# Performance work log

Hardware: AMD Instinct MI355X
Metric: run time of the kernel (lower is better)

## Reference

```python
import jax, jax.numpy as jnp
import numpy as np

K = 9          # neighbors per node (loop=False)
BN_EPS = 1e-5  # BatchNorm2d eps


def setup_inputs() -> dict:
    key = jax.random.key(0)
    k1, k2, k3 = jax.random.split(key, 3)
    B, C, H, W_ = 16, 384, 32, 32
    x = jax.random.normal(k1, (B, C, H, W_), dtype=jnp.float32)
    # GCNConv linear weight (PyG stores [out, in]; y = x @ W.T) and bias
    Wg = jax.random.normal(k2, (C, C), dtype=jnp.float32) / np.sqrt(C)
    bg = jax.random.normal(k3, (C,), dtype=jnp.float32) * 0.02
    gamma = jnp.ones((C,), dtype=jnp.float32)
    beta = jnp.zeros((C,), dtype=jnp.float32)
    return {"x": x, "Wg": Wg, "bg": bg, "gamma": gamma, "beta": beta}


def _knn_indices(xn):
    # xn: [B, N, C] -> neighbor indices [B, N, K] (self excluded)
    sq = jnp.sum(xn * xn, axis=-1)                       # [B, N]
    d = sq[:, :, None] + sq[:, None, :] - 2.0 * jnp.einsum("bnc,bmc->bnm", xn, xn)
    N = xn.shape[1]
    d = d + jnp.eye(N, dtype=xn.dtype) * jnp.finfo(xn.dtype).max  # exclude self
    _, nbr = jax.lax.top_k(-d, K)                        # [B, N, K]
    return nbr


def reference(x, Wg, bg, gamma, beta):
    B, C, H, W_ = x.shape
    N = H * W_
    BN_nodes = B * N
    shortcut = x

    # Flatten to nodes: [B*N, C]
    xn = jnp.transpose(x, (0, 2, 3, 1)).reshape(B, N, C)

    # Per-graph kNN in feature space (PyG knn_graph, flow source_to_target:
    # edges from neighbor (src) to query node (dst))
    nbr = _knn_indices(xn)                                # [B, N, K]
    offs = (jnp.arange(B) * N)[:, None, None]             # [B,1,1]
    src = (nbr + offs).reshape(-1)                        # [B*N*K]
    dst = jnp.broadcast_to(jnp.arange(N)[None, :, None] + offs, (B, N, K)).reshape(-1)

    # GCNConv: add self loops, symmetric normalization
    loops = jnp.arange(BN_nodes)
    src = jnp.concatenate([src, loops])
    dst = jnp.concatenate([dst, loops])

    xw = xn.reshape(BN_nodes, C) @ Wg.T                   # node-wise linear

    deg = jax.ops.segment_sum(jnp.ones_like(dst, dtype=xw.dtype), dst, num_segments=BN_nodes)
    dinv = jax.lax.rsqrt(deg)                             # deg >= 1 due to self loops
    norm = dinv[src] * dinv[dst]                          # [E]

    out = jax.ops.segment_sum(norm[:, None] * xw[src], dst, num_segments=BN_nodes) + bg

    # Back to B x C x H x W
    out = jnp.transpose(out.reshape(B, H, W_, C), (0, 3, 1, 2))

    # BatchNorm2d (training-mode batch statistics, biased variance)
    mu = jnp.mean(out, axis=(0, 2, 3), keepdims=True)
    var = jnp.mean((out - mu) ** 2, axis=(0, 2, 3), keepdims=True)
    out = gamma[None, :, None, None] * (out - mu) * jax.lax.rsqrt(var + BN_EPS) + beta[None, :, None, None]

    # GELU + residual (drop_path = 0 -> identity)
    out = jax.nn.gelu(out) + shortcut
    return out
```

## Files before the change

kernel.cpp:

```cpp
#include <hip/hip_runtime.h>
#include <math.h>

#define B_ 16
#define C_ 384
#define N_ 1024
#define K_ 9

typedef _Float16 f16x8 __attribute__((ext_vector_type(8)));
typedef _Float16 f16x4 __attribute__((ext_vector_type(4)));
typedef float f32x4 __attribute__((ext_vector_type(4)));
typedef unsigned long long u64;

__device__ __forceinline__ void gld_lds16(const void* g, void* l) {
  __builtin_amdgcn_global_load_lds((const __attribute__((address_space(1))) void*)g,
                                   (__attribute__((address_space(3))) void*)l, 16, 0, 0);
}

__global__ void k_cvt(const float* __restrict__ x, ushort* __restrict__ xhT,
                      ushort* __restrict__ xlT) {
  const int bid = blockIdx.x;
  const int ct = bid % 12;
  const int nt = (bid / 12) & 15;
  const int b = bid / 192;
  const int c0 = ct * 32, n0 = nt * 64;
  __shared__ float ld[32 * 65];
  const int t = threadIdx.x;
  {
    const int c = t >> 3, n8 = (t & 7) * 8;
    const float* src = x + ((size_t)(b * C_ + c0 + c) * N_ + n0 + n8);
    float4 v0 = *(const float4*)src;
    float4 v1 = *(const float4*)(src + 4);
    float vv[8] = {v0.x, v0.y, v0.z, v0.w, v1.x, v1.y, v1.z, v1.w};
#pragma unroll
    for (int j = 0; j < 8; ++j) ld[c * 65 + n8 + j] = vv[j];
  }
  __syncthreads();
  {
    const int n = t >> 2, c8 = (t & 3) * 8;
    f16x8 hv, lv;
#pragma unroll
    for (int j = 0; j < 8; ++j) {
      float v = ld[(c8 + j) * 65 + n];
      _Float16 h = (_Float16)v;
      _Float16 l = (_Float16)(v - (float)h);
      hv[j] = h;
      lv[j] = l;
    }
    const size_t off = (size_t)(b * N_ + n0 + n) * C_ + c0 + c8;
    *(f16x8*)(xhT + off) = hv;
    *(f16x8*)(xlT + off) = lv;
  }
}

__global__ void k_cvtw(const float* __restrict__ Wg, ushort* __restrict__ WgH,
                       ushort* __restrict__ WgL) {
  const int i = (blockIdx.x * 256 + threadIdx.x) * 4;
  float4 v = *(const float4*)(Wg + i);
  float vv[4] = {v.x, v.y, v.z, v.w};
  f16x4 hv, lv;
#pragma unroll
  for (int j = 0; j < 4; ++j) {
    _Float16 h = (_Float16)vv[j];
    hv[j] = h;
    lv[j] = (_Float16)(vv[j] - (float)h);
  }
  *(f16x4*)(WgH + i) = hv;
  *(f16x4*)(WgL + i) = lv;
}

__global__ void k_sq1(const float* __restrict__ x, double* __restrict__ part) {
  const int bid = blockIdx.x;
  const int b = bid >> 6, q = (bid >> 2) & 15, nt = bid & 3;
  const int n = nt * 256 + threadIdx.x;
  const float* xb = x + ((size_t)b * C_ + q * 24) * N_ + n;
  double s = 0.0;
#pragma unroll 4
  for (int c = 0; c < 24; ++c) {
    float v = xb[(size_t)c * N_];
    s = fma((double)v, (double)v, s);
  }
  part[((size_t)b * 16 + q) * N_ + n] = s;
}

__global__ void k_sq2(const double* __restrict__ part, float* __restrict__ sq) {
  const int idx = blockIdx.x * blockDim.x + threadIdx.x;
  const int b = idx >> 10, n = idx & 1023;
  const double* p = part + (size_t)b * 16 * N_ + n;
  double s = 0.0;
#pragma unroll
  for (int q = 0; q < 16; ++q) s += p[(size_t)q * N_];
  sq[idx] = (float)s;
}

__global__ __launch_bounds__(256, 2) void k_gram(const ushort* __restrict__ xhT,
                                                 const ushort* __restrict__ xlT,
                                                 const float* __restrict__ sq,
                                                 float* __restrict__ D, int base_b, int nb) {
  const int bid = blockIdx.x;
  int b_local, pid;
  if (nb >= 8) {
    const int x = bid & 7, j = bid >> 3, grp = nb >> 3;
    b_local = x * grp + (j >> 6);
    pid = j & 63;
  } else {
    b_local = bid >> 6;
    pid = bid & 63;
  }
  const int b = base_b + b_local;
  const int rt = pid >> 3, mt = pid & 7;
  const int n0 = rt * 128, m0 = mt * 128;

  __shared__ alignas(16) char sm[2][32768];
  const int t = threadIdx.x;
  const int lane = t & 63, wid = t >> 6, quad = lane >> 4, lrow = lane & 15;
  const int wr = wid >> 1, wc = wid & 1;
  const int lrow4 = lane >> 2, lpos = lane & 3;

  const char* src = (const char*)((wid & 1) ? xlT : xhT) +
                    (size_t)(b * N_ + ((wid >> 1) ? m0 : n0)) * C_ * 2;

  f32x4 acc[4][4];
#pragma unroll
  for (int mi = 0; mi < 4; ++mi)
#pragma unroll
    for (int ni = 0; ni < 4; ++ni) acc[mi][ni] = (f32x4){0.f, 0.f, 0.f, 0.f};

  auto stage = [&](int it) {
    char* dst = sm[it & 1] + wid * 8192;
    const int ktB = it * 64;
#pragma unroll
    for (int i = 0; i < 8; ++i) {
      const int row = i * 16 + lrow4;
      const int swz = lpos ^ ((row >> 1) & 3);
      gld_lds16(src + (size_t)row * 768 + ktB + swz * 16, dst + i * 1024 + lane * 16);
    }
  };

  stage(0);
  for (int it = 0; it < 12; ++it) {
    __syncthreads();
    if (it < 11) stage(it + 1);
    const char* smb = sm[it & 1];
    f16x8 ah[4], al[4];
#pragma unroll
    for (int mi = 0; mi < 4; ++mi) {
      const int row = wr * 64 + mi * 16 + lrow;
      const int off = row * 64 + (quad ^ ((row >> 1) & 3)) * 16;
      ah[mi] = *(const f16x8*)(smb + off);
      al[mi] = *(const f16x8*)(smb + 8192 + off);
    }
#pragma unroll
    for (int ni = 0; ni < 4; ++ni) {
      const int row = wc * 64 + ni * 16 + lrow;
      const int off = row * 64 + (quad ^ ((row >> 1) & 3)) * 16;
      f16x8 bh = *(const f16x8*)(smb + 16384 + off);
      f16x8 bl = *(const f16x8*)(smb + 24576 + off);
#pragma unroll
      for (int mi = 0; mi < 4; ++mi) {
        acc[mi][ni] = __builtin_amdgcn_mfma_f32_16x16x32_f16(ah[mi], bh, acc[mi][ni], 0, 0, 0);
        acc[mi][ni] = __builtin_amdgcn_mfma_f32_16x16x32_f16(al[mi], bh, acc[mi][ni], 0, 0, 0);
        acc[mi][ni] = __builtin_amdgcn_mfma_f32_16x16x32_f16(ah[mi], bl, acc[mi][ni], 0, 0, 0);
      }
    }
  }

  const float* sqb = sq + b * N_;
  float sqm[4];
#pragma unroll
  for (int ni = 0; ni < 4; ++ni) sqm[ni] = sqb[m0 + wc * 64 + ni * 16 + lrow];
  float sqn_[4][4];
#pragma unroll
  for (int mi = 0; mi < 4; ++mi)
#pragma unroll
    for (int r = 0; r < 4; ++r) sqn_[mi][r] = sqb[n0 + wr * 64 + mi * 16 + quad * 4 + r];

  float* Db = D + (size_t)b_local * N_ * N_;
#pragma unroll
  for (int mi = 0; mi < 4; ++mi)
#pragma unroll
    for (int ni = 0; ni < 4; ++ni)
#pragma unroll
      for (int r = 0; r < 4; ++r) {
        const int ng = n0 + wr * 64 + mi * 16 + quad * 4 + r;
        const int mg = m0 + wc * 64 + ni * 16 + lrow;
        float d = fmaf(-2.f, acc[mi][ni][r], sqn_[mi][r] + sqm[ni]);
        if (ng == mg) d = 3.402823466e38f;
        Db[(size_t)ng * N_ + mg] = d;
      }
}

__device__ __forceinline__ void ce2f(float& a, float& b) {
  float lo = fminf(a, b), hi = fmaxf(a, b);
  a = lo;
  b = hi;
}

__global__ __launch_bounds__(256) void k_scan(const float* __restrict__ D,
                                              int* __restrict__ nbr, int base_node) {
  const int t = threadIdx.x;
  const int lane = t & 63, wid = t >> 6;
  const int g = lane >> 5;
  const int ll = lane & 31;
  const int nl = blockIdx.x * 8 + wid * 2 + g;
  const float* row = D + (size_t)nl * N_ + ll * 32;
  float v[32];
#pragma unroll
  for (int i = 0; i < 8; ++i) {
    float4 q = *(const float4*)(row + i * 4);
    v[i * 4 + 0] = q.x;
    v[i * 4 + 1] = q.y;
    v[i * 4 + 2] = q.z;
    v[i * 4 + 3] = q.w;
  }
  float key[9];
#pragma unroll
  for (int k = 0; k < 9; ++k) key[k] = 3.402823466e38f;
#pragma unroll
  for (int j = 0; j < 32; ++j) {
    key[8] = fminf(key[8], v[j]);
#pragma unroll
    for (int s = 8; s >= 1; --s) ce2f(key[s - 1], key[s]);
  }
#pragma unroll
  for (int lvl = 1; lvl < 32; lvl <<= 1) {
    float pk[9];
#pragma unroll
    for (int k = 0; k < 9; ++k) pk[k] = __shfl_xor(key[k], lvl, 64);
    float m[9];
#pragma unroll
    for (int k = 0; k < 9; ++k) m[k] = fminf(key[k], pk[8 - k]);
    ce2f(m[0], m[8]);
    ce2f(m[1], m[5]); ce2f(m[2], m[6]); ce2f(m[3], m[7]); ce2f(m[4], m[8]);
    ce2f(m[1], m[3]); ce2f(m[2], m[4]); ce2f(m[5], m[7]); ce2f(m[6], m[8]);
    ce2f(m[1], m[2]); ce2f(m[3], m[4]); ce2f(m[5], m[6]); ce2f(m[7], m[8]);
#pragma unroll
    for (int k = 0; k < 9; ++k) key[k] = m[k];
  }
  const float v9 = key[8];
  int c_lt = 0;
#pragma unroll
  for (int k = 0; k < 8; ++k) c_lt += (key[k] < v9) ? 1 : 0;

  unsigned lt_mask = 0u, eq_mask = 0u;
#pragma unroll
  for (int j = 0; j < 32; ++j) {
    lt_mask |= (v[j] < v9) ? (1u << j) : 0u;
    eq_mask |= (v[j] == v9) ? (1u << j) : 0u;
  }
  const int lt_cnt = __popc(lt_mask), eq_cnt = __popc(eq_mask);
  int packed = lt_cnt | (eq_cnt << 16);
  int run = packed;
#pragma unroll
  for (int off = 1; off < 32; off <<= 1) {
    int q = __shfl_up(run, off, 32);
    if (ll >= off) run += q;
  }
  const int pref = run - packed;
  const int lt_pref = pref & 0xFFFF, eq_pref = pref >> 16;

  int* np = nbr + (size_t)(base_node + nl) * K_;
  int slot = lt_pref;
  unsigned m = lt_mask;
  while (m) {
    int j = __builtin_ctz(m);
    m &= m - 1;
    np[slot++] = ll * 32 + j;
  }
  slot = c_lt + eq_pref;
  m = eq_mask;
  while (m && slot < 9) {
    int j = __builtin_ctz(m);
    m &= m - 1;
    np[slot++] = ll * 32 + j;
  }
}

__global__ __launch_bounds__(256, 3) void k_xw(const ushort* __restrict__ xhT,
                                               const ushort* __restrict__ xlT,
                                               const ushort* __restrict__ WgH,
                                               const ushort* __restrict__ WgL,
                                               float* __restrict__ xw) {
  const int bid = blockIdx.x;
  const int xcd = bid & 7, j = bid >> 3;
  const int pair = xcd * 16 + j / 6;
  const int ct = j % 6;
  const int b = pair >> 3, nt = pair & 7;
  const int co0 = ct * 64, n0 = nt * 128;
  __shared__ alignas(16) char sm[2][24576];
  const int t = threadIdx.x;
  const int lane = t & 63, wid = t >> 6, quad = lane >> 4, lrow = lane & 15;
  const int wr = wid >> 1, wc = wid & 1;
  const int lrow4 = lane >> 2, lpos = lane & 3;

  f32x4 acc[2][4];
#pragma unroll
  for (int mi = 0; mi < 2; ++mi)
#pragma unroll
    for (int ni = 0; ni < 4; ++ni) acc[mi][ni] = (f32x4){0.f, 0.f, 0.f, 0.f};

  const char* asrc[2] = {(const char*)(WgH + (size_t)co0 * C_),
                         (const char*)(WgL + (size_t)co0 * C_)};
  const char* bsrc[2] = {(const char*)(xhT + (size_t)(b * N_ + n0) * C_),
                         (const char*)(xlT + (size_t)(b * N_ + n0) * C_)};

  auto stage = [&](int it) {
    char* dst = sm[it & 1];
    const int ktB = it * 64;
#pragma unroll
    for (int i = 0; i < 6; ++i) {
      const int c = wid * 6 + i;
      const char* src;
      int base, row;
      if (c < 8) {
        const int arr = c >> 2, sub = c & 3;
        src = asrc[arr];
        base = arr * 4096 + sub * 1024;
        row = sub * 16 + lrow4;
      } else {
        const int cc = c - 8, arr = cc >> 3, sub = cc & 7;
        src = bsrc[arr];
        base = 8192 + arr * 8192 + sub * 1024;
        row = sub * 16 + lrow4;
      }
      const int swz = lpos ^ ((row >> 1) & 3);
      gld_lds16(src + (size_t)row * 768 + ktB + swz * 16, dst + base + lane * 16);
    }
  };

  stage(0);
  for (int it = 0; it < 12; ++it) {
    __syncthreads();
    if (it < 11) stage(it + 1);
    const char* smb = sm[it & 1];
    f16x8 bh[4], bl[4];
#pragma unroll
    for (int ni = 0; ni < 4; ++ni) {
      const int row = wr * 64 + ni * 16 + lrow;
      const int off = row * 64 + (quad ^ ((row >> 1) & 3)) * 16;
      bh[ni] = *(const f16x8*)(smb + 8192 + off);
      bl[ni] = *(const f16x8*)(smb + 16384 + off);
    }
#pragma unroll
    for (int mi = 0; mi < 2; ++mi) {
      const int row = wc * 32 + mi * 16 + lrow;
      const int off = row * 64 + (quad ^ ((row >> 1) & 3)) * 16;
      f16x8 ah = *(const f16x8*)(smb + off);
      f16x8 al = *(const f16x8*)(smb + 4096 + off);
#pragma unroll
      for (int ni = 0; ni < 4; ++ni) {
        acc[mi][ni] = __builtin_amdgcn_mfma_f32_16x16x32_f16(ah, bh[ni], acc[mi][ni], 0, 0, 0);
        acc[mi][ni] = __builtin_amdgcn_mfma_f32_16x16x32_f16(al, bh[ni], acc[mi][ni], 0, 0, 0);
        acc[mi][ni] = __builtin_amdgcn_mfma_f32_16x16x32_f16(ah, bl[ni], acc[mi][ni], 0, 0, 0);
      }
    }
  }
#pragma unroll
  for (int mi = 0; mi < 2; ++mi)
#pragma unroll
    for (int ni = 0; ni < 4; ++ni)
#pragma unroll
      for (int r = 0; r < 4; ++r) {
        const int c_g = co0 + wc * 32 + mi * 16 + quad * 4 + r;
        const int n_g = n0 + wr * 64 + ni * 16 + lrow;
        xw[((size_t)b * C_ + c_g) * N_ + n_g] = acc[mi][ni][r];
      }
}

__global__ __launch_bounds__(256) void k_agg(const float* __restrict__ xw,
                                             const int* __restrict__ nbr,
                                             const float* __restrict__ bg,
                                             float* __restrict__ out,
                                             float* __restrict__ stats) {
  const int ct = blockIdx.x % (C_ / 8);
  const int b = blockIdx.x / (C_ / 8);
  const int c0 = ct * 8;
  __shared__ alignas(16) int nb_l[N_ * K_];
  __shared__ alignas(16) float row_l[8][N_ + 4];
  __shared__ float red[2][8][4];
  const int tid = threadIdx.x;
  const int4* gp = (const int4*)(nbr + (size_t)b * N_ * K_);
  int4* lp = (int4*)nb_l;
  for (int t = tid; t < N_ * K_ / 4; t += 256) lp[t] = gp[t];
  for (int t = tid; t < 8 * (N_ / 4); t += 256) {
    const int j = t >> 8, n4 = t & 255;
    float4 v = ((const float4*)(xw + ((size_t)(b * C_ + c0 + j)) * N_))[n4];
    *(float4*)&row_l[j][n4 * 4] = v;
  }
  __syncthreads();
  float bgc[8];
#pragma unroll
  for (int j = 0; j < 8; ++j) bgc[j] = bg[c0 + j];
  float s1[8], s2[8];
#pragma unroll
  for (int j = 0; j < 8; ++j) {
    s1[j] = 0.f;
    s2[j] = 0.f;
  }
  float* outb = out + ((size_t)b * C_ + c0) * N_;
#pragma unroll
  for (int s = 0; s < 4; ++s) {
    const int n = tid + 256 * s;
    const int* nn_ = &nb_l[n * K_];
    int idx[K_];
#pragma unroll
    for (int k = 0; k < K_; ++k) idx[k] = nn_[k];
    float a[8];
#pragma unroll
    for (int j = 0; j < 8; ++j) a[j] = row_l[j][n];
#pragma unroll
    for (int k = 0; k < K_; ++k) {
      const int m = idx[k];
#pragma unroll
      for (int j = 0; j < 8; ++j) a[j] += row_l[j][m];
    }
#pragma unroll
    for (int j = 0; j < 8; ++j) {
      float y = fmaf(a[j], 0.099999994f, bgc[j]);
      outb[(size_t)j * N_ + n] = y;
      s1[j] += y;
      s2[j] = fmaf(y, y, s2[j]);
    }
  }
#pragma unroll
  for (int off = 32; off > 0; off >>= 1)
#pragma unroll
    for (int j = 0; j < 8; ++j) {
      s1[j] += __shfl_down(s1[j], off, 64);
      s2[j] += __shfl_down(s2[j], off, 64);
    }
  const int lane = tid & 63, wid = tid >> 6;
  if (lane == 0)
#pragma unroll
    for (int j = 0; j < 8; ++j) {
      red[0][j][wid] = s1[j];
      red[1][j][wid] = s2[j];
    }
  __syncthreads();
  if (tid < 16) {
    const int j = tid & 7, which = tid >> 3;
    float v = red[which][j][0] + red[which][j][1] + red[which][j][2] + red[which][j][3];
    atomicAdd(&stats[which * C_ + c0 + j], v);
  }
}

__global__ void k_bn(const float* __restrict__ x, const float* __restrict__ gamma,
                     const float* __restrict__ beta, const float* __restrict__ stats,
                     float* __restrict__ out) {
  const int f = blockIdx.x * blockDim.x + threadIdx.x;
  const int e = f * 4;
  const int c = (e >> 10) % C_;
  const float inv = 1.f / 16384.f;
  const float mu = stats[c] * inv;
  const float var = fmaf(-mu, mu, stats[C_ + c] * inv);
  const float sc = gamma[c] * rsqrtf(var + 1e-5f);
  const float sh = fmaf(-mu, sc, beta[c]);
  float4 y = ((const float4*)out)[f];
  float4 xv = ((const float4*)x)[f];
  auto gl = [](float z) {
    float z3 = z * z * z;
    float t = 0.7978845608028654f * fmaf(0.044715f, z3, z);
    float th = tanhf(t);
    return 0.5f * z * (1.f + th);
  };
  float4 o;
  o.x = gl(fmaf(y.x, sc, sh)) + xv.x;
  o.y = gl(fmaf(y.y, sc, sh)) + xv.y;
  o.z = gl(fmaf(y.z, sc, sh)) + xv.z;
  o.w = gl(fmaf(y.w, sc, sh)) + xv.w;
  ((float4*)out)[f] = o;
}

extern "C" void kernel_launch(void* const* d_in, const int* in_sizes, int n_in,
                              void* d_out, int out_size, void* d_ws, size_t ws_size,
                              hipStream_t stream) {
  const float* x = (const float*)d_in[0];
  const float* Wg = (const float*)d_in[1];
  const float* bg = (const float*)d_in[2];
  const float* gamma = (const float*)d_in[3];
  const float* beta = (const float*)d_in[4];
  float* out = (float*)d_out;

  int nb;
  if (ws_size >= 94000000) nb = 16;
  else if (ws_size >= 60500000) nb = 8;
  else nb = 4;

  char* ws = (char*)d_ws;
  ushort* xhT = (ushort*)ws;
  ushort* xlT = (ushort*)(ws + 12582912);
  ushort* WgH = (ushort*)(ws + 25165824);
  ushort* WgL = (ushort*)(ws + 25460736);
  float* sq = (float*)(ws + 25755648);
  float* Dbuf = (float*)(ws + 25821184);
  float* xw = (float*)(ws + 25821184);
  double* sqpart = (double*)(ws + 25821184);
  size_t dreg = (size_t)nb * 4194304;
  if (dreg < 25165824) dreg = 25165824;
  int* nbr = (int*)(ws + 25821184 + dreg);
  float* stats = (float*)(ws + 25821184 + dreg + 589824);

  hipMemsetAsync(stats, 0, 2 * C_ * sizeof(float), stream);
  k_cvt<<<3072, 256, 0, stream>>>(x, xhT, xlT);
  k_cvtw<<<144, 256, 0, stream>>>(Wg, WgH, WgL);
  k_sq1<<<1024, 256, 0, stream>>>(x, sqpart);
  k_sq2<<<64, 256, 0, stream>>>(sqpart, sq);
  for (int r = 0; r < B_ / nb; ++r) {
    k_gram<<<nb * 64, 256, 0, stream>>>(xhT, xlT, sq, Dbuf, r * nb, nb);
    k_scan<<<nb * 128, 256, 0, stream>>>(Dbuf, nbr, r * nb * N_);
  }
  k_xw<<<768, 256, 0, stream>>>(xhT, xlT, WgH, WgL, xw);
  k_agg<<<B_ * (C_ / 8), 256, 0, stream>>>(xw, nbr, bg, out, stats);
  k_bn<<<6144, 256, 0, stream>>>(x, gamma, beta, stats, out);
}
```

Baseline: 219.5 us.

## Fuse kNN top-k selection into gram kernel epilogue with per-tile partial merge

Instead of writing the full dense NxN distance matrix to global memory and rescanning it, the gram kernel now transposes its MFMA outputs, stages each 128x128 distance tile in LDS with a swizzle, and computes a per-tile top-9 per query row there. It writes packed (monotone-float, index) 64-bit candidates, 72 per node, and a small merge kernel reduces those to the final 9 neighbours. This removes the large global write and read of the distance matrix, and the batch-chunking loop now always processes all 16 graphs in one launch. The cost is extra LDS work and a serial top-k in the gram epilogue. The merge kernel runs only 64 blocks, so it has low parallelism.

```diff
diff --git a/kernel.cpp b/kernel.cpp
--- a/kernel.cpp
+++ b/kernel.cpp
@@ -92,10 +92,22 @@
   sq[idx] = (float)s;
 }
 
+__device__ __forceinline__ void ce2f(float& a, float& b) {
+  float lo = fminf(a, b), hi = fmaxf(a, b);
+  a = lo;
+  b = hi;
+}
+__device__ __forceinline__ void ce9u(u64& a, u64& b) {
+  u64 lo = a < b ? a : b;
+  u64 hi = a < b ? b : a;
+  a = lo;
+  b = hi;
+}
+
 __global__ __launch_bounds__(256, 2) void k_gram(const ushort* __restrict__ xhT,
                                                  const ushort* __restrict__ xlT,
                                                  const float* __restrict__ sq,
-                                                 float* __restrict__ D, int base_b, int nb) {
+                                                 u64* __restrict__ part, int base_b, int nb) {
   const int bid = blockIdx.x;
   int b_local, pid;
   if (nb >= 8) {
@@ -157,75 +169,72 @@
       f16x8 bl = *(const f16x8*)(smb + 24576 + off);
 #pragma unroll
       for (int mi = 0; mi < 4; ++mi) {
-        acc[mi][ni] = __builtin_amdgcn_mfma_f32_16x16x32_f16(ah[mi], bh, acc[mi][ni], 0, 0, 0);
-        acc[mi][ni] = __builtin_amdgcn_mfma_f32_16x16x32_f16(al[mi], bh, acc[mi][ni], 0, 0, 0);
-        acc[mi][ni] = __builtin_amdgcn_mfma_f32_16x16x32_f16(ah[mi], bl, acc[mi][ni], 0, 0, 0);
+        acc[mi][ni] = __builtin_amdgcn_mfma_f32_16x16x32_f16(bh, ah[mi], acc[mi][ni], 0, 0, 0);
+        acc[mi][ni] = __builtin_amdgcn_mfma_f32_16x16x32_f16(bh, al[mi], acc[mi][ni], 0, 0, 0);
+        acc[mi][ni] = __builtin_amdgcn_mfma_f32_16x16x32_f16(bl, ah[mi], acc[mi][ni], 0, 0, 0);
       }
     }
   }
+  __syncthreads();
 
   const float* sqb = sq + b * N_;
-  float sqm[4];
-#pragma unroll
-  for (int ni = 0; ni < 4; ++ni) sqm[ni] = sqb[m0 + wc * 64 + ni * 16 + lrow];
-  float sqn_[4][4];
-#pragma unroll
-  for (int mi = 0; mi < 4; ++mi)
-#pragma unroll
-    for (int r = 0; r < 4; ++r) sqn_[mi][r] = sqb[n0 + wr * 64 + mi * 16 + quad * 4 + r];
-
-  float* Db = D + (size_t)b_local * N_ * N_;
-#pragma unroll
-  for (int mi = 0; mi < 4; ++mi)
-#pragma unroll
-    for (int ni = 0; ni < 4; ++ni)
+  float sqm_[4][4];
+#pragma unroll
+  for (int ni = 0; ni < 4; ++ni)
+#pragma unroll
+    for (int r = 0; r < 4; ++r) sqm_[ni][r] = sqb[m0 + wc * 64 + ni * 16 + quad * 4 + r];
+  float sqq_[4];
+#pragma unroll
+  for (int mi = 0; mi < 4; ++mi) sqq_[mi] = sqb[n0 + wr * 64 + mi * 16 + lrow];
+
+  float* smf = (float*)sm;
+#pragma unroll
+  for (int mi = 0; mi < 4; ++mi) {
+    const int qL = wr * 64 + mi * 16 + lrow;
+    const int qG = n0 + qL;
+#pragma unroll
+    for (int ni = 0; ni < 4; ++ni) {
+      const int tc = wc * 16 + ni * 4 + quad;
+      const int stv = tc ^ (qL & 31);
+      f32x4 dv;
 #pragma unroll
       for (int r = 0; r < 4; ++r) {
-        const int ng = n0 + wr * 64 + mi * 16 + quad * 4 + r;
-        const int mg = m0 + wc * 64 + ni * 16 + lrow;
-        float d = fmaf(-2.f, acc[mi][ni][r], sqn_[mi][r] + sqm[ni]);
-        if (ng == mg) d = 3.402823466e38f;
-        Db[(size_t)ng * N_ + mg] = d;
+        const int mG = m0 + wc * 64 + ni * 16 + quad * 4 + r;
+        float d = fmaf(-2.f, acc[mi][ni][r], sqq_[mi] + sqm_[ni][r]);
+        if (mG == qG) d = 3.402823466e38f;
+        dv[r] = d;
       }
-}
-
-__device__ __forceinline__ void ce2f(float& a, float& b) {
-  float lo = fminf(a, b), hi = fmaxf(a, b);
-  a = lo;
-  b = hi;
-}
-
-__global__ __launch_bounds__(256) void k_scan(const float* __restrict__ D,
-                                              int* __restrict__ nbr, int base_node) {
-  const int t = threadIdx.x;
-  const int lane = t & 63, wid = t >> 6;
-  const int g = lane >> 5;
-  const int ll = lane & 31;
-  const int nl = blockIdx.x * 8 + wid * 2 + g;
-  const float* row = D + (size_t)nl * N_ + ll * 32;
-  float v[32];
-#pragma unroll
-  for (int i = 0; i < 8; ++i) {
-    float4 q = *(const float4*)(row + i * 4);
-    v[i * 4 + 0] = q.x;
-    v[i * 4 + 1] = q.y;
-    v[i * 4 + 2] = q.z;
-    v[i * 4 + 3] = q.w;
+      *(f32x4*)(smf + qL * 128 + stv * 4) = dv;
+    }
+  }
+  __syncthreads();
+
+  const int qsel = wid * 32 + (lane & 31);
+  const int half = lane >> 5;
+  float v[64];
+#pragma unroll
+  for (int i = 0; i < 16; ++i) {
+    const int tc = half * 16 + i;
+    const int stv = tc ^ (qsel & 31);
+    f32x4 q4 = *(const f32x4*)(smf + qsel * 128 + stv * 4);
+    v[i * 4 + 0] = q4[0];
+    v[i * 4 + 1] = q4[1];
+    v[i * 4 + 2] = q4[2];
+    v[i * 4 + 3] = q4[3];
   }
   float key[9];
 #pragma unroll
   for (int k = 0; k < 9; ++k) key[k] = 3.402823466e38f;
 #pragma unroll
-  for (int j = 0; j < 32; ++j) {
+  for (int j = 0; j < 64; ++j) {
     key[8] = fminf(key[8], v[j]);
 #pragma unroll
     for (int s = 8; s >= 1; --s) ce2f(key[s - 1], key[s]);
   }
-#pragma unroll
-  for (int lvl = 1; lvl < 32; lvl <<= 1) {
+  {
     float pk[9];
 #pragma unroll
-    for (int k = 0; k < 9; ++k) pk[k] = __shfl_xor(key[k], lvl, 64);
+    for (int k = 0; k < 9; ++k) pk[k] = __shfl_xor(key[k], 32, 64);
     float m[9];
 #pragma unroll
     for (int k = 0; k < 9; ++k) m[k] = fminf(key[k], pk[8 - k]);
@@ -241,38 +250,58 @@
 #pragma unroll
   for (int k = 0; k < 8; ++k) c_lt += (key[k] < v9) ? 1 : 0;
 
-  unsigned lt_mask = 0u, eq_mask = 0u;
-#pragma unroll
-  for (int j = 0; j < 32; ++j) {
-    lt_mask |= (v[j] < v9) ? (1u << j) : 0u;
-    eq_mask |= (v[j] == v9) ? (1u << j) : 0u;
-  }
-  const int lt_cnt = __popc(lt_mask), eq_cnt = __popc(eq_mask);
-  int packed = lt_cnt | (eq_cnt << 16);
-  int run = packed;
-#pragma unroll
-  for (int off = 1; off < 32; off <<= 1) {
-    int q = __shfl_up(run, off, 32);
-    if (ll >= off) run += q;
-  }
-  const int pref = run - packed;
-  const int lt_pref = pref & 0xFFFF, eq_pref = pref >> 16;
-
+  u64 lt_mask = 0ull, eq_mask = 0ull;
+#pragma unroll
+  for (int j = 0; j < 64; ++j) {
+    lt_mask |= (v[j] < v9) ? (1ull << j) : 0ull;
+    eq_mask |= (v[j] == v9) ? (1ull << j) : 0ull;
+  }
+  const int ltc = __popcll(lt_mask), eqc = __popcll(eq_mask);
+  const int packed = ltc | (eqc << 16);
+  const int other = __shfl_xor(packed, 32, 64);
+  const int lt_pref = half ? (other & 0xFFFF) : 0;
+  const int eq_pref = half ? (other >> 16) : 0;
+
+  u64* pp = part + ((size_t)(b_local * N_ + n0 + qsel) * 8 + mt) * 9;
+  int slot = lt_pref;
+  u64 msk = lt_mask;
+  while (msk) {
+    const int j = __builtin_ctzll(msk);
+    msk &= msk - 1;
+    const int mL = half * 64 + j;
+    const int stv = (mL >> 2) ^ (qsel & 31);
+    const float val = smf[qsel * 128 + stv * 4 + (mL & 3)];
+    unsigned fb = __float_as_uint(val);
+    unsigned mono = (fb >> 31) ? ~fb : (fb | 0x80000000u);
+    pp[slot++] = ((u64)mono << 32) | (unsigned)(m0 + mL);
+  }
+  unsigned fb9 = __float_as_uint(v9);
+  unsigned mono9 = (fb9 >> 31) ? ~fb9 : (fb9 | 0x80000000u);
+  slot = c_lt + eq_pref;
+  msk = eq_mask;
+  while (msk && slot < 9) {
+    const int j = __builtin_ctzll(msk);
+    msk &= msk - 1;
+    pp[slot++] = ((u64)mono9 << 32) | (unsigned)(m0 + half * 64 + j);
+  }
+}
+
+__global__ void k_mrg(const u64* __restrict__ part, int* __restrict__ nbr, int base_node) {
+  const int nl = blockIdx.x * 256 + threadIdx.x;
+  const u64* p = part + (size_t)nl * 72;
+  u64 key[9];
+#pragma unroll
+  for (int k = 0; k < 9; ++k) key[k] = ~0ull;
+#pragma unroll 4
+  for (int j = 0; j < 72; ++j) {
+    u64 kk = p[j];
+    key[8] = key[8] < kk ? key[8] : kk;
+#pragma unroll
+    for (int s = 8; s >= 1; --s) ce9u(key[s - 1], key[s]);
+  }
   int* np = nbr + (size_t)(base_node + nl) * K_;
-  int slot = lt_pref;
-  unsigned m = lt_mask;
-  while (m) {
-    int j = __builtin_ctz(m);
-    m &= m - 1;
-    np[slot++] = ll * 32 + j;
-  }
-  slot = c_lt + eq_pref;
-  m = eq_mask;
-  while (m && slot < 9) {
-    int j = __builtin_ctz(m);
-    m &= m - 1;
-    np[slot++] = ll * 32 + j;
-  }
+#pragma unroll
+  for (int k = 0; k < 9; ++k) np[k] = (int)(unsigned)(key[k] & 0xFFFFFFFFu);
 }
 
 __global__ __launch_bounds__(256, 3) void k_xw(const ushort* __restrict__ xhT,
@@ -480,10 +509,7 @@
   const float* beta = (const float*)d_in[4];
   float* out = (float*)d_out;
 
-  int nb;
-  if (ws_size >= 94000000) nb = 16;
-  else if (ws_size >= 60500000) nb = 8;
-  else nb = 4;
+  const int nb = 16;
 
   char* ws = (char*)d_ws;
   ushort* xhT = (ushort*)ws;
@@ -491,11 +517,10 @@
   ushort* WgH = (ushort*)(ws + 25165824);
   ushort* WgL = (ushort*)(ws + 25460736);
   float* sq = (float*)(ws + 25755648);
-  float* Dbuf = (float*)(ws + 25821184);
+  u64* part = (u64*)(ws + 25821184);
   float* xw = (float*)(ws + 25821184);
   double* sqpart = (double*)(ws + 25821184);
-  size_t dreg = (size_t)nb * 4194304;
-  if (dreg < 25165824) dreg = 25165824;
+  size_t dreg = 25165824;
   int* nbr = (int*)(ws + 25821184 + dreg);
   float* stats = (float*)(ws + 25821184 + dreg + 589824);
 
@@ -504,10 +529,8 @@
   k_cvtw<<<144, 256, 0, stream>>>(Wg, WgH, WgL);
   k_sq1<<<1024, 256, 0, stream>>>(x, sqpart);
   k_sq2<<<64, 256, 0, stream>>>(sqpart, sq);
-  for (int r = 0; r < B_ / nb; ++r) {
-    k_gram<<<nb * 64, 256, 0, stream>>>(xhT, xlT, sq, Dbuf, r * nb, nb);
-    k_scan<<<nb * 128, 256, 0, stream>>>(Dbuf, nbr, r * nb * N_);
-  }
+  k_gram<<<nb * 64, 256, 0, stream>>>(xhT, xlT, sq, part, 0, nb);
+  k_mrg<<<nb * 4, 256, 0, stream>>>(part, nbr, 0);
   k_xw<<<768, 256, 0, stream>>>(xhT, xlT, WgH, WgL, xw);
   k_agg<<<B_ * (C_ / 8), 256, 0, stream>>>(xw, nbr, bg, out, stats);
   k_bn<<<6144, 256, 0, stream>>>(x, gamma, beta, stats, out);
```

Result: no change. 220.9 us (+0.7%).
